# Kernel optimization log

Measured on AMD Instinct MI355X. Metric: run time of the kernel, lower is better.

The kernel has to match this reference:

```python
import jax, jax.numpy as jnp
import numpy as np
from jax import lax

V, E, H = 32000, 128, 128
B, T = 8, 512


def setup_inputs() -> dict:
    key = jax.random.key(0)
    ks = jax.random.split(key, 12)
    s = 1.0 / np.sqrt(H)
    return {
        "x": jax.random.randint(ks[0], (B, T), 0, V, dtype=jnp.int32),
        "embedding": jax.random.normal(ks[1], (V, E), jnp.float32) * s,
        "W_ih0": jax.random.normal(ks[2], (H, E), jnp.float32) * s,
        "W_hh0": jax.random.normal(ks[3], (H, H), jnp.float32) * s,
        "b_ih0": jax.random.normal(ks[4], (H,), jnp.float32) * s,
        "b_hh0": jax.random.normal(ks[5], (H,), jnp.float32) * s,
        "W_ih1": jax.random.normal(ks[6], (H, H), jnp.float32) * s,
        "W_hh1": jax.random.normal(ks[7], (H, H), jnp.float32) * s,
        "b_ih1": jax.random.normal(ks[8], (H,), jnp.float32) * s,
        "b_hh1": jax.random.normal(ks[9], (H,), jnp.float32) * s,
        "fc_W": jax.random.normal(ks[10], (V, H), jnp.float32) * s,
        "fc_b": jax.random.normal(ks[11], (V,), jnp.float32) * s,
    }


def _rnn_layer(x_tbe, W_ih, W_hh, b_ih, b_hh):
    # x_tbe: [T, B, in]. Precompute input contribution once (big GEMM), then scan.
    pre = jnp.einsum("tbe,he->tbh", x_tbe, W_ih) + b_ih + b_hh  # [T,B,H]

    def step(h, p):
        h = jnp.tanh(p + h @ W_hh.T)
        return h, h

    h0 = jnp.zeros((x_tbe.shape[1], W_hh.shape[0]), x_tbe.dtype)
    _, ys = lax.scan(step, h0, pre)
    return ys  # [T,B,H]


def reference(x, embedding, W_ih0, W_hh0, b_ih0, b_hh0,
              W_ih1, W_hh1, b_ih1, b_hh1, fc_W, fc_b):
    emb = embedding[x]                    # [B,T,E] gather
    h = jnp.transpose(emb, (1, 0, 2))     # [T,B,E] time-major for scan
    h = _rnn_layer(h, W_ih0, W_hh0, b_ih0, b_hh0)
    h = _rnn_layer(h, W_ih1, W_hh1, b_ih1, b_hh1)
    logits = jnp.einsum("tbh,vh->btv", h, fc_W) + fc_b  # [B,T,V]
    return logits
```

## Files before the change

kernel.cpp:

```cpp
#include <hip/hip_runtime.h>
#include <hip/hip_bf16.h>

typedef __attribute__((ext_vector_type(4))) float f32x4;
typedef __attribute__((ext_vector_type(4))) int   i32x4;
typedef __attribute__((ext_vector_type(8))) short s16x8;
typedef __attribute__((ext_vector_type(4))) unsigned short u16x4;
typedef __attribute__((ext_vector_type(2))) unsigned int  u32x2;
typedef __attribute__((ext_vector_type(2))) unsigned long long u64x2;

#define T_ 512
#define B_ 8
#define H_ 128
#define V_ 32000

#define WS_PRE0   0u
#define WS_H1B    (2u<<20)
#define WS_FCWB   (3u<<20)
#define WS_PIH    (11u<<20)
#define WS_FLAGS  (15u<<20)

__device__ __forceinline__ unsigned short f2b(float f) {
  unsigned int u = __float_as_uint(f);
  u = (u + 0x7FFFu + ((u >> 16) & 1u)) >> 16;
  return (unsigned short)u;
}

__device__ __forceinline__ float hsum4(f32x4 v) { return (v.x + v.y) + (v.z + v.w); }

__device__ __forceinline__ float tanh_fast(float x) {
  float e = __expf(2.f * x);
  return 1.f - 2.f * __builtin_amdgcn_rcpf(e + 1.f);
}

__device__ __forceinline__ f32x4 tanh4(f32x4 v) {
  f32x4 r;
  r.x = tanh_fast(v.x); r.y = tanh_fast(v.y);
  r.z = tanh_fast(v.z); r.w = tanh_fast(v.w);
  return r;
}

__device__ __forceinline__ u32x2 pk4(f32x4 v) {
  unsigned int a, b;
  asm("v_cvt_pk_bf16_f32 %0, %1, %2" : "=v"(a) : "v"(v.x), "v"(v.y));
  asm("v_cvt_pk_bf16_f32 %0, %1, %2" : "=v"(b) : "v"(v.z), "v"(v.w));
  u32x2 r; r.x = a; r.y = b; return r;
}

__device__ __forceinline__ void lds_barrier() {
  asm volatile("s_waitcnt lgkmcnt(0)\n\ts_barrier" ::: "memory");
}

__device__ __forceinline__ void st_u64(unsigned long long* p, unsigned long long v) {
  __hip_atomic_store(p, v, __ATOMIC_RELAXED, __HIP_MEMORY_SCOPE_AGENT);
}
__device__ __forceinline__ unsigned long long ld_u64(const unsigned long long* p) {
  return __hip_atomic_load(p, __ATOMIC_RELAXED, __HIP_MEMORY_SCOPE_AGENT);
}

#define MFMA16(A, B, C) __builtin_amdgcn_mfma_f32_16x16x32_bf16((A), (B), (C), 0, 0, 0)

__global__ __launch_bounds__(128) void pre_kernel(const float* __restrict__ emb,
                                                  const int* __restrict__ x,
                                                  const float* __restrict__ W,
                                                  const float* __restrict__ b1,
                                                  const float* __restrict__ b2,
                                                  float* __restrict__ out) {
  const int tid = threadIdx.x;
  __shared__ alignas(16) float lds_in[H_];
  f32x4 w[32];
#pragma unroll
  for (int r = 0; r < 32; ++r) w[r] = *(const f32x4*)(W + tid * H_ + 4 * r);
  const float bsum = b1[tid] + b2[tid];
  const int m0 = blockIdx.x * 16;

  auto src_row = [&](int m) -> const float* {
    int t = m >> 3, b = m & 7;
    int tok = x[(b << 9) + t];
    return emb + (size_t)tok * H_;
  };

  float stage = src_row(m0)[tid];
  for (int rr = 0; rr < 16; ++rr) {
    const int m = m0 + rr;
    lds_in[tid] = stage;
    __syncthreads();
    if (rr + 1 < 16) stage = src_row(m0 + rr + 1)[tid];
    f32x4 acc4 = {0.f, 0.f, 0.f, 0.f};
#pragma unroll
    for (int r = 0; r < 32; ++r) {
      f32x4 hv = *(const f32x4*)(lds_in + 4 * r);
      acc4 = __builtin_elementwise_fma(hv, w[r], acc4);
    }
    out[m * H_ + tid] = hsum4(acc4) + bsum;
    __syncthreads();
  }
}

__global__ __launch_bounds__(512) __attribute__((amdgpu_waves_per_eu(2, 2)))
void fused_scan5(const float* __restrict__ pre0,
                 const float* __restrict__ W_hh0,
                 const float* __restrict__ W_ih1,
                 const float* __restrict__ W_hh1,
                 const float* __restrict__ b_ih1,
                 const float* __restrict__ b_hh1,
                 unsigned short* __restrict__ h1b,
                 unsigned long long* __restrict__ pih_g,
                 unsigned int* __restrict__ prog1,
                 const float* __restrict__ fcw_src,
                 unsigned short* __restrict__ fcw_dst) {
  const int bid = blockIdx.x;
  const int tid = threadIdx.x;

  if (bid >= 2) {
    int idx = (bid - 2) * 512 + tid;
    const int stride = 64 * 512;
    const int n4 = V_ * H_ / 4;
    for (int c = idx; c < n4; c += stride) {
      f32x4 v = ((const f32x4*)fcw_src)[c];
      u16x4 o; o.x = f2b(v.x); o.y = f2b(v.y); o.z = f2b(v.z); o.w = f2b(v.w);
      ((u16x4*)fcw_dst)[c] = o;
    }
    return;
  }

  __shared__ unsigned short hl[2][16][136];
  const int wv = tid >> 6, lane = tid & 63;
  const int n = lane & 15, g = lane >> 4;
  const int nn = (n < 8) ? n : 7;
  for (int i = tid; i < 2 * 16 * 136; i += 512) ((unsigned short*)hl)[i] = 0;

  if (bid == 0) {
    const bool is0 = wv < 4;
    const int w = wv & 3, m0 = w * 32;
    const float* Wm = is0 ? W_hh0 : W_ih1;
    s16x8 whi[2][4], wlo[2][4];
#pragma unroll
    for (int hf = 0; hf < 2; ++hf)
#pragma unroll
      for (int kt = 0; kt < 4; ++kt) {
        const float* src = Wm + (m0 + hf * 16 + n) * H_ + kt * 32 + g * 8;
        s16x8 hi, lo;
#pragma unroll
        for (int j = 0; j < 8; ++j) {
          float v = src[j];
          unsigned short hb = f2b(v);
          hi[j] = (short)hb;
          lo[j] = (short)f2b(v - __uint_as_float(((unsigned int)hb) << 16));
        }
        whi[hf][kt] = hi; wlo[hf][kt] = lo;
      }
    f32x4 c0b = {0.f,0.f,0.f,0.f}, c1b = {0.f,0.f,0.f,0.f};
    if (!is0) {
      c0b = *(const f32x4*)(b_ih1 + m0 + g * 4) + *(const f32x4*)(b_hh1 + m0 + g * 4);
      c1b = *(const f32x4*)(b_ih1 + m0 + 16 + g * 4) + *(const f32x4*)(b_hh1 + m0 + 16 + g * 4);
    }
    f32x4 fif[4][2];
    if (is0) {
#pragma unroll
      for (int k = 0; k < 4; ++k) {
        fif[k][0] = *(const f32x4*)(pre0 + (k * B_ + nn) * H_ + m0 + g * 4);
        fif[k][1] = *(const f32x4*)(pre0 + (k * B_ + nn) * H_ + m0 + 16 + g * 4);
      }
    }
    __syncthreads();

    for (int base = 0; base < T_; base += 4) {
#pragma unroll
      for (int k = 0; k < 4; ++k) {
        const int s = base + k;
        const int rd = (k + 1) & 1, wr = k & 1;
        const unsigned short* hb = &hl[rd][n][0];
        s16x8 b0 = *(const s16x8*)(hb + g * 8);
        s16x8 b1 = *(const s16x8*)(hb + 32 + g * 8);
        s16x8 b2 = *(const s16x8*)(hb + 64 + g * 8);
        s16x8 b3 = *(const s16x8*)(hb + 96 + g * 8);
        if (is0) {
          f32x4 aH0 = fif[k][0], aL0 = {0.f,0.f,0.f,0.f};
          f32x4 aH1 = fif[k][1], aL1 = {0.f,0.f,0.f,0.f};
          aH0 = MFMA16(whi[0][0], b0, aH0); aL0 = MFMA16(wlo[0][0], b0, aL0);
          aH0 = MFMA16(whi[0][1], b1, aH0); aL0 = MFMA16(wlo[0][1], b1, aL0);
          aH0 = MFMA16(whi[0][2], b2, aH0); aL0 = MFMA16(wlo[0][2], b2, aL0);
          aH0 = MFMA16(whi[0][3], b3, aH0); aL0 = MFMA16(wlo[0][3], b3, aL0);
          aH1 = MFMA16(whi[1][0], b0, aH1); aL1 = MFMA16(wlo[1][0], b0, aL1);
          aH1 = MFMA16(whi[1][1], b1, aH1); aL1 = MFMA16(wlo[1][1], b1, aL1);
          aH1 = MFMA16(whi[1][2], b2, aH1); aL1 = MFMA16(wlo[1][2], b2, aL1);
          aH1 = MFMA16(whi[1][3], b3, aH1); aL1 = MFMA16(wlo[1][3], b3, aL1);
          f32x4 v0 = tanh4(aH0 + aL0), v1 = tanh4(aH1 + aL1);
          *(u32x2*)&hl[wr][n][m0 + g * 4] = pk4(v0);
          *(u32x2*)&hl[wr][n][m0 + 16 + g * 4] = pk4(v1);
          int sp = s + 4; if (sp > T_ - 1) sp = T_ - 1;
          fif[k][0] = *(const f32x4*)(pre0 + (sp * B_ + nn) * H_ + m0 + g * 4);
          fif[k][1] = *(const f32x4*)(pre0 + (sp * B_ + nn) * H_ + m0 + 16 + g * 4);
        } else {
          if (k == 0 && base >= 4 && lane == 0)
            __hip_atomic_fetch_add(prog1, 4u, __ATOMIC_RELEASE, __HIP_MEMORY_SCOPE_AGENT);
          if (s >= 1) {
            f32x4 v0 = c0b, v1 = c1b;
            v0 = MFMA16(whi[0][0], b0, v0); v1 = MFMA16(whi[1][0], b0, v1);
            v0 = MFMA16(whi[0][1], b1, v0); v1 = MFMA16(whi[1][1], b1, v1);
            v0 = MFMA16(whi[0][2], b2, v0); v1 = MFMA16(whi[1][2], b2, v1);
            v0 = MFMA16(whi[0][3], b3, v0); v1 = MFMA16(whi[1][3], b3, v1);
            u64x2 u0 = __builtin_bit_cast(u64x2, v0);
            u64x2 u1 = __builtin_bit_cast(u64x2, v1);
            unsigned long long* p0 = pih_g + ((size_t)((s - 1) * 8 + 2 * w) * 64 + lane) * 2;
            st_u64(p0, u0.x); st_u64(p0 + 1, u0.y);
            unsigned long long* p1 = pih_g + ((size_t)((s - 1) * 8 + 2 * w + 1) * 64 + lane) * 2;
            st_u64(p1, u1.x); st_u64(p1 + 1, u1.y);
          }
        }
        lds_barrier();
      }
    }
    if (!is0) {
      const unsigned short* hb = &hl[1][n][0];
      s16x8 b0 = *(const s16x8*)(hb + g * 8);
      s16x8 b1 = *(const s16x8*)(hb + 32 + g * 8);
      s16x8 b2 = *(const s16x8*)(hb + 64 + g * 8);
      s16x8 b3 = *(const s16x8*)(hb + 96 + g * 8);
      f32x4 v0 = c0b, v1 = c1b;
      v0 = MFMA16(whi[0][0], b0, v0); v1 = MFMA16(whi[1][0], b0, v1);
      v0 = MFMA16(whi[0][1], b1, v0); v1 = MFMA16(whi[1][1], b1, v1);
      v0 = MFMA16(whi[0][2], b2, v0); v1 = MFMA16(whi[1][2], b2, v1);
      v0 = MFMA16(whi[0][3], b3, v0); v1 = MFMA16(whi[1][3], b3, v1);
      u64x2 u0 = __builtin_bit_cast(u64x2, v0);
      u64x2 u1 = __builtin_bit_cast(u64x2, v1);
      unsigned long long* p0 = pih_g + ((size_t)(511 * 8 + 2 * w) * 64 + lane) * 2;
      st_u64(p0, u0.x); st_u64(p0 + 1, u0.y);
      unsigned long long* p1 = pih_g + ((size_t)(511 * 8 + 2 * w + 1) * 64 + lane) * 2;
      st_u64(p1, u1.x); st_u64(p1 + 1, u1.y);
      if (lane == 0)
        __hip_atomic_fetch_add(prog1, 16u, __ATOMIC_RELEASE, __HIP_MEMORY_SCOPE_AGENT);
    }
  } else {
    const int m0 = wv * 16;
    s16x8 whi[4], wlo[4];
#pragma unroll
    for (int kt = 0; kt < 4; ++kt) {
      const float* src = W_hh1 + (m0 + n) * H_ + kt * 32 + g * 8;
      s16x8 hi, lo;
#pragma unroll
      for (int j = 0; j < 8; ++j) {
        float v = src[j];
        unsigned short hb = f2b(v);
        hi[j] = (short)hb;
        lo[j] = (short)f2b(v - __uint_as_float(((unsigned int)hb) << 16));
      }
      whi[kt] = hi; wlo[kt] = lo;
    }
    __syncthreads();

    auto ld_pih = [&](int step) -> f32x4 {
      const unsigned long long* p = pih_g + ((size_t)(step * 8 + wv) * 64 + lane) * 2;
      u64x2 u; u.x = ld_u64(p); u.y = ld_u64(p + 1);
      return __builtin_bit_cast(f32x4, u);
    };
    while (__hip_atomic_load(prog1, __ATOMIC_ACQUIRE, __HIP_MEMORY_SCOPE_AGENT) < 20u)
      __builtin_amdgcn_s_sleep(2);
    f32x4 fif[4];
#pragma unroll
    for (int k = 0; k < 4; ++k) fif[k] = ld_pih(k);

    for (int base = 0; base < T_; base += 4) {
      if (base + 4 < T_) {
        const unsigned int t = 4u * (unsigned)(base + 9);
        while (__hip_atomic_load(prog1, __ATOMIC_ACQUIRE, __HIP_MEMORY_SCOPE_AGENT) < t)
          __builtin_amdgcn_s_sleep(2);
      }
#pragma unroll
      for (int k = 0; k < 4; ++k) {
        const int j = base + k;
        const int rd = (k + 1) & 1, wr = k & 1;
        const unsigned short* hb = &hl[rd][n][0];
        s16x8 b0 = *(const s16x8*)(hb + g * 8);
        s16x8 b1 = *(const s16x8*)(hb + 32 + g * 8);
        s16x8 b2 = *(const s16x8*)(hb + 64 + g * 8);
        s16x8 b3 = *(const s16x8*)(hb + 96 + g * 8);
        f32x4 aH = fif[k], aL = {0.f,0.f,0.f,0.f};
        aH = MFMA16(whi[0], b0, aH); aL = MFMA16(wlo[0], b0, aL);
        aH = MFMA16(whi[1], b1, aH); aL = MFMA16(wlo[1], b1, aL);
        aH = MFMA16(whi[2], b2, aH); aL = MFMA16(wlo[2], b2, aL);
        aH = MFMA16(whi[3], b3, aH); aL = MFMA16(wlo[3], b3, aL);
        f32x4 v = tanh4(aH + aL);
        u32x2 o = pk4(v);
        *(u32x2*)&hl[wr][n][m0 + g * 4] = o;
        if (n < 8) *(u32x2*)(h1b + ((j * B_ + n) << 7) + m0 + g * 4) = o;
        if (j + 4 < T_) fif[k] = ld_pih(j + 4);
        lds_barrier();
      }
    }
  }
}

__device__ __forceinline__ int swz(int row, int cc) {
  return row * 256 + ((cc ^ (row & 7)) << 4);
}

__global__ __launch_bounds__(256) void final_gemm5(const unsigned short* __restrict__ fcWb,
                                                   const unsigned short* __restrict__ h1b,
                                                   const float* __restrict__ bias,
                                                   float* __restrict__ out) {
  const int bid = blockIdx.x;
  const int x   = bid & 7;
  const int jb  = bid >> 3;
  const int mt  = jb & 31;
  const int ntl = jb >> 5;
  const int nt  = x * 32 + ntl;
  if (nt >= 250) return;

  __shared__ alignas(16) char smem[33792];
  const int tid = threadIdx.x;
  const int bb = mt >> 2, tb = mt & 3;
  const int t0 = tb << 7;
  const int v0 = nt << 7;
  const int lane = tid & 63, wvv = tid >> 6;

  const char* gW = (const char*)fcWb + (size_t)v0 * 256;
#pragma unroll
  for (int it = 0; it < 8; ++it) {
    int cidx = it * 256 + tid;
    i32x4 vw = *(const i32x4*)(gW + cidx * 16);
    *(i32x4*)(smem + swz(cidx >> 4, cidx & 15)) = vw;
  }
  __syncthreads();

  const int l15 = lane & 15, lg = lane >> 4;
  f32x4 acc[8][2] = {};
#pragma unroll
  for (int kk = 0; kk < 4; ++kk) {
    const int cc = kk * 4 + lg;
    s16x8 a[8], bfr[2];
#pragma unroll
    for (int vf = 0; vf < 8; ++vf)
      a[vf] = *(const s16x8*)(smem + swz(vf * 16 + l15, cc));
#pragma unroll
    for (int mf = 0; mf < 2; ++mf) {
      int trow = t0 + wvv * 32 + mf * 16 + l15;
      bfr[mf] = *(const s16x8*)(h1b + (size_t)((trow << 3) + bb) * H_ + kk * 32 + lg * 8);
    }
#pragma unroll
    for (int vf = 0; vf < 8; ++vf)
#pragma unroll
      for (int mf = 0; mf < 2; ++mf)
        acc[vf][mf] = __builtin_amdgcn_mfma_f32_16x16x32_bf16(a[vf], bfr[mf], acc[vf][mf], 0, 0, 0);
  }

#pragma unroll
  for (int vf = 0; vf < 8; ++vf) {
    f32x4 bv = *(const f32x4*)(bias + v0 + vf * 16 + (lg << 2));
#pragma unroll
    for (int mf = 0; mf < 2; ++mf) acc[vf][mf] += bv;
  }

  float* tbf = (float*)smem;
#pragma unroll
  for (int p = 0; p < 2; ++p) {
    __syncthreads();
#pragma unroll
    for (int q = 0; q < 4; ++q) {
      const int vf = p * 4 + q;
#pragma unroll
      for (int mf = 0; mf < 2; ++mf) {
        int t = wvv * 32 + mf * 16 + l15;
        int vl = q * 16 + lg * 4;
        *(f32x4*)(tbf + t * 66 + vl) = acc[vf][mf];
      }
    }
    __syncthreads();
#pragma unroll
    for (int it = 0; it < 8; ++it) {
      int row = it * 16 + (tid >> 4);
      int col = (tid & 15) * 4;
      f32x4 val = *(const f32x4*)(tbf + row * 66 + col);
      const size_t off = (size_t)((bb << 9) + t0 + row) * V_ + v0 + p * 64 + col;
      __builtin_nontemporal_store(val, (f32x4*)(out + off));
    }
  }
}

extern "C" void kernel_launch(void* const* d_in, const int* in_sizes, int n_in,
                              void* d_out, int out_size, void* d_ws, size_t ws_size,
                              hipStream_t stream) {
  const int*   x     = (const int*)d_in[0];
  const float* emb   = (const float*)d_in[1];
  const float* W_ih0 = (const float*)d_in[2];
  const float* W_hh0 = (const float*)d_in[3];
  const float* b_ih0 = (const float*)d_in[4];
  const float* b_hh0 = (const float*)d_in[5];
  const float* W_ih1 = (const float*)d_in[6];
  const float* W_hh1 = (const float*)d_in[7];
  const float* b_ih1 = (const float*)d_in[8];
  const float* b_hh1 = (const float*)d_in[9];
  const float* fc_W  = (const float*)d_in[10];
  const float* fc_b  = (const float*)d_in[11];
  float* out = (float*)d_out;

  char* ws = (char*)d_ws;
  float*              pre0  = (float*)(ws + WS_PRE0);
  unsigned short*     h1b   = (unsigned short*)(ws + WS_H1B);
  unsigned short*     fcWb  = (unsigned short*)(ws + WS_FCWB);
  unsigned long long* pih_g = (unsigned long long*)(ws + WS_PIH);
  unsigned int*       prog1 = (unsigned int*)(ws + WS_FLAGS);

  hipMemsetAsync(ws + WS_FLAGS, 0, 4096, stream);
  pre_kernel<<<256, 128, 0, stream>>>(emb, x, W_ih0, b_ih0, b_hh0, pre0);
  fused_scan5<<<66, 512, 0, stream>>>(pre0, W_hh0, W_ih1, W_hh1, b_ih1, b_hh1,
                                      h1b, pih_g, prog1, fc_W, fcWb);
  final_gemm5<<<8192, 256, 0, stream>>>(fcWb, h1b, fc_b, out);
}
```

Before: 475.4 us.

## Split recurrent scan into three pipelined blocks and convert fc weights in GEMM

The fused scan kernel now runs three blocks. Block 0 computes layer-0 recurrence alone with all 8 waves, block 1 computes the layer-1 input projection from h0 in global memory, and block 2 runs the layer-1 recurrence, all chained through acquire/release progress flags checked every 8 steps. This removes the layer-1 projection from the critical serial path of layer 0 and halves the per-wave MFMA chain. The separate fc_W fp32-to-bf16 conversion blocks are removed and the conversion moves into the final GEMM's tile load, which trades a workspace pass for redundant per-tile conversion across the 32 M-tiles.

```diff
diff --git a/kernel.cpp b/kernel.cpp
--- a/kernel.cpp
+++ b/kernel.cpp
@@ -6,7 +6,6 @@
 typedef __attribute__((ext_vector_type(8))) short s16x8;
 typedef __attribute__((ext_vector_type(4))) unsigned short u16x4;
 typedef __attribute__((ext_vector_type(2))) unsigned int  u32x2;
-typedef __attribute__((ext_vector_type(2))) unsigned long long u64x2;
 
 #define T_ 512
 #define B_ 8
@@ -15,9 +14,9 @@
 
 #define WS_PRE0   0u
 #define WS_H1B    (2u<<20)
-#define WS_FCWB   (3u<<20)
-#define WS_PIH    (11u<<20)
-#define WS_FLAGS  (15u<<20)
+#define WS_H0G    (3u<<20)
+#define WS_PIH    (4u<<20)
+#define WS_FLAGS  (8u<<20)
 
 __device__ __forceinline__ unsigned short f2b(float f) {
   unsigned int u = __float_as_uint(f);
@@ -50,14 +49,15 @@
   asm volatile("s_waitcnt lgkmcnt(0)\n\ts_barrier" ::: "memory");
 }
 
-__device__ __forceinline__ void st_u64(unsigned long long* p, unsigned long long v) {
-  __hip_atomic_store(p, v, __ATOMIC_RELAXED, __HIP_MEMORY_SCOPE_AGENT);
-}
-__device__ __forceinline__ unsigned long long ld_u64(const unsigned long long* p) {
-  return __hip_atomic_load(p, __ATOMIC_RELAXED, __HIP_MEMORY_SCOPE_AGENT);
+__device__ __forceinline__ unsigned int ld_flag_acq(const unsigned int* p) {
+  return __hip_atomic_load(p, __ATOMIC_ACQUIRE, __HIP_MEMORY_SCOPE_AGENT);
 }
 
 #define MFMA16(A, B, C) __builtin_amdgcn_mfma_f32_16x16x32_bf16((A), (B), (C), 0, 0, 0)
+
+__device__ __forceinline__ int swz(int row, int cc) {
+  return row * 256 + ((cc ^ (row & 7)) << 4);
+}
 
 __global__ __launch_bounds__(128) void pre_kernel(const float* __restrict__ emb,
                                                   const int* __restrict__ x,
@@ -96,143 +96,167 @@
   }
 }
 
+#define S0_STEP(S, FIF) { \
+  const int s_ = (S); \
+  const int rd = (s_ + 1) & 1, wr = s_ & 1; \
+  const unsigned short* hb = &hl[rd][n][0]; \
+  s16x8 b0 = *(const s16x8*)(hb + g * 8); \
+  s16x8 b1 = *(const s16x8*)(hb + 32 + g * 8); \
+  s16x8 b2 = *(const s16x8*)(hb + 64 + g * 8); \
+  s16x8 b3 = *(const s16x8*)(hb + 96 + g * 8); \
+  f32x4 ha = MFMA16(whi[0], b0, FIF); \
+  f32x4 hc = MFMA16(whi[2], b2, z4); \
+  f32x4 la = MFMA16(wlo[0], b0, z4); \
+  f32x4 lb = MFMA16(wlo[2], b2, z4); \
+  ha = MFMA16(whi[1], b1, ha); \
+  hc = MFMA16(whi[3], b3, hc); \
+  la = MFMA16(wlo[1], b1, la); \
+  lb = MFMA16(wlo[3], b3, lb); \
+  f32x4 v = tanh4((ha + hc) + (la + lb)); \
+  u32x2 o = pk4(v); \
+  *(u32x2*)&hl[wr][n][m0 + g * 4] = o; \
+  if (n < 8) *(u32x2*)(h0g + ((s_ * 8 + n) << 7) + m0 + g * 4) = o; \
+  int sp = s_ + 4; if (sp > T_ - 1) sp = T_ - 1; \
+  if ((s_ & 7) == 7) { \
+    asm volatile("s_waitcnt vmcnt(0)" ::: "memory"); \
+    (FIF) = *(const f32x4*)(pre0 + ((sp * 8 + nn) << 7) + m0 + g * 4); \
+    lds_barrier(); \
+    if (tid == 0) __hip_atomic_fetch_add(prog0, 8u, __ATOMIC_RELEASE, __HIP_MEMORY_SCOPE_AGENT); \
+  } else { \
+    (FIF) = *(const f32x4*)(pre0 + ((sp * 8 + nn) << 7) + m0 + g * 4); \
+    lds_barrier(); \
+  } \
+}
+
+#define S1_STEP(JJ, FB) { \
+  const int j_ = (JJ); \
+  f32x4 aa = MFMA16(whi[0], FB[0], biasD); \
+  f32x4 ab = MFMA16(whi[2], FB[2], z4); \
+  aa = MFMA16(whi[1], FB[1], aa); \
+  ab = MFMA16(whi[3], FB[3], ab); \
+  f32x4 v = aa + ab; \
+  *(f32x4*)(pih_gf + (size_t)(j_ * 8 + wv) * 64 + n * 4 + g) = v; \
+  if ((j_ & 7) == 7) { \
+    asm volatile("s_waitcnt vmcnt(0)" ::: "memory"); \
+    lds_barrier(); \
+    if (tid == 0) __hip_atomic_fetch_add(prog1, 8u, __ATOMIC_RELEASE, __HIP_MEMORY_SCOPE_AGENT); \
+  } \
+  int jp = j_ + 4; \
+  if (jp < T_) { \
+    const unsigned short* hsrc = h0g + ((jp * 8 + nn) << 7); \
+    FB[0] = *(const s16x8*)(hsrc + g * 8); \
+    FB[1] = *(const s16x8*)(hsrc + 32 + g * 8); \
+    FB[2] = *(const s16x8*)(hsrc + 64 + g * 8); \
+    FB[3] = *(const s16x8*)(hsrc + 96 + g * 8); \
+  } \
+}
+
+#define S2_STEP(J, PF) { \
+  const int j_ = (J); \
+  const int rd = (j_ + 1) & 1, wr = j_ & 1; \
+  const unsigned short* hb = &hl[rd][n][0]; \
+  s16x8 b0 = *(const s16x8*)(hb + g * 8); \
+  s16x8 b1 = *(const s16x8*)(hb + 32 + g * 8); \
+  s16x8 b2 = *(const s16x8*)(hb + 64 + g * 8); \
+  s16x8 b3 = *(const s16x8*)(hb + 96 + g * 8); \
+  f32x4 ha = MFMA16(whi[0], b0, PF); \
+  f32x4 hc = MFMA16(whi[2], b2, z4); \
+  f32x4 la = MFMA16(wlo[0], b0, z4); \
+  f32x4 lb = MFMA16(wlo[2], b2, z4); \
+  ha = MFMA16(whi[1], b1, ha); \
+  hc = MFMA16(whi[3], b3, hc); \
+  la = MFMA16(wlo[1], b1, la); \
+  lb = MFMA16(wlo[3], b3, lb); \
+  f32x4 v = tanh4((ha + hc) + (la + lb)); \
+  u32x2 o = pk4(v); \
+  *(u32x2*)&hl[wr][n][m0 + g * 4] = o; \
+  if (n < 8) *(u32x2*)(h1b + ((j_ * 8 + n) << 7) + m0 + g * 4) = o; \
+  int jp = j_ + 4; \
+  if (jp < T_) (PF) = *(const f32x4*)(pih_gf + (size_t)(jp * 8 + wv) * 64 + n * 4 + g); \
+  lds_barrier(); \
+}
+
 __global__ __launch_bounds__(512) __attribute__((amdgpu_waves_per_eu(2, 2)))
-void fused_scan5(const float* __restrict__ pre0,
+void fused_scan6(const float* __restrict__ pre0,
                  const float* __restrict__ W_hh0,
                  const float* __restrict__ W_ih1,
                  const float* __restrict__ W_hh1,
                  const float* __restrict__ b_ih1,
                  const float* __restrict__ b_hh1,
+                 unsigned short* __restrict__ h0g,
+                 float* __restrict__ pih_raw,
                  unsigned short* __restrict__ h1b,
-                 unsigned long long* __restrict__ pih_g,
-                 unsigned int* __restrict__ prog1,
-                 const float* __restrict__ fcw_src,
-                 unsigned short* __restrict__ fcw_dst) {
+                 unsigned int* __restrict__ prog0,
+                 unsigned int* __restrict__ prog1) {
   const int bid = blockIdx.x;
   const int tid = threadIdx.x;
-
-  if (bid >= 2) {
-    int idx = (bid - 2) * 512 + tid;
-    const int stride = 64 * 512;
-    const int n4 = V_ * H_ / 4;
-    for (int c = idx; c < n4; c += stride) {
-      f32x4 v = ((const f32x4*)fcw_src)[c];
-      u16x4 o; o.x = f2b(v.x); o.y = f2b(v.y); o.z = f2b(v.z); o.w = f2b(v.w);
-      ((u16x4*)fcw_dst)[c] = o;
-    }
-    return;
-  }
-
-  __shared__ unsigned short hl[2][16][136];
   const int wv = tid >> 6, lane = tid & 63;
   const int n = lane & 15, g = lane >> 4;
   const int nn = (n < 8) ? n : 7;
+  const int m0 = wv * 16;
+  const f32x4 z4 = {0.f, 0.f, 0.f, 0.f};
+  f32x4* pih_gf = (f32x4*)pih_raw;
+
+  __shared__ unsigned short hl[2][16][136];
   for (int i = tid; i < 2 * 16 * 136; i += 512) ((unsigned short*)hl)[i] = 0;
 
   if (bid == 0) {
-    const bool is0 = wv < 4;
-    const int w = wv & 3, m0 = w * 32;
-    const float* Wm = is0 ? W_hh0 : W_ih1;
-    s16x8 whi[2][4], wlo[2][4];
-#pragma unroll
-    for (int hf = 0; hf < 2; ++hf)
-#pragma unroll
-      for (int kt = 0; kt < 4; ++kt) {
-        const float* src = Wm + (m0 + hf * 16 + n) * H_ + kt * 32 + g * 8;
-        s16x8 hi, lo;
-#pragma unroll
-        for (int j = 0; j < 8; ++j) {
-          float v = src[j];
-          unsigned short hb = f2b(v);
-          hi[j] = (short)hb;
-          lo[j] = (short)f2b(v - __uint_as_float(((unsigned int)hb) << 16));
-        }
-        whi[hf][kt] = hi; wlo[hf][kt] = lo;
+    s16x8 whi[4], wlo[4];
+#pragma unroll
+    for (int kt = 0; kt < 4; ++kt) {
+      const float* src = W_hh0 + (m0 + n) * H_ + kt * 32 + g * 8;
+      s16x8 hi, lo;
+#pragma unroll
+      for (int j = 0; j < 8; ++j) {
+        float v = src[j];
+        unsigned short hb16 = f2b(v);
+        hi[j] = (short)hb16;
+        lo[j] = (short)f2b(v - __uint_as_float(((unsigned int)hb16) << 16));
       }
-    f32x4 c0b = {0.f,0.f,0.f,0.f}, c1b = {0.f,0.f,0.f,0.f};
-    if (!is0) {
-      c0b = *(const f32x4*)(b_ih1 + m0 + g * 4) + *(const f32x4*)(b_hh1 + m0 + g * 4);
-      c1b = *(const f32x4*)(b_ih1 + m0 + 16 + g * 4) + *(const f32x4*)(b_hh1 + m0 + 16 + g * 4);
-    }
-    f32x4 fif[4][2];
-    if (is0) {
-#pragma unroll
-      for (int k = 0; k < 4; ++k) {
-        fif[k][0] = *(const f32x4*)(pre0 + (k * B_ + nn) * H_ + m0 + g * 4);
-        fif[k][1] = *(const f32x4*)(pre0 + (k * B_ + nn) * H_ + m0 + 16 + g * 4);
-      }
-    }
-    __syncthreads();
-
+      whi[kt] = hi; wlo[kt] = lo;
+    }
+    f32x4 f0 = *(const f32x4*)(pre0 + ((0 * 8 + nn) << 7) + m0 + g * 4);
+    f32x4 f1 = *(const f32x4*)(pre0 + ((1 * 8 + nn) << 7) + m0 + g * 4);
+    f32x4 f2 = *(const f32x4*)(pre0 + ((2 * 8 + nn) << 7) + m0 + g * 4);
+    f32x4 f3 = *(const f32x4*)(pre0 + ((3 * 8 + nn) << 7) + m0 + g * 4);
+    __syncthreads();
     for (int base = 0; base < T_; base += 4) {
-#pragma unroll
-      for (int k = 0; k < 4; ++k) {
-        const int s = base + k;
-        const int rd = (k + 1) & 1, wr = k & 1;
-        const unsigned short* hb = &hl[rd][n][0];
-        s16x8 b0 = *(const s16x8*)(hb + g * 8);
-        s16x8 b1 = *(const s16x8*)(hb + 32 + g * 8);
-        s16x8 b2 = *(const s16x8*)(hb + 64 + g * 8);
-        s16x8 b3 = *(const s16x8*)(hb + 96 + g * 8);
-        if (is0) {
-          f32x4 aH0 = fif[k][0], aL0 = {0.f,0.f,0.f,0.f};
-          f32x4 aH1 = fif[k][1], aL1 = {0.f,0.f,0.f,0.f};
-          aH0 = MFMA16(whi[0][0], b0, aH0); aL0 = MFMA16(wlo[0][0], b0, aL0);
-          aH0 = MFMA16(whi[0][1], b1, aH0); aL0 = MFMA16(wlo[0][1], b1, aL0);
-          aH0 = MFMA16(whi[0][2], b2, aH0); aL0 = MFMA16(wlo[0][2], b2, aL0);
-          aH0 = MFMA16(whi[0][3], b3, aH0); aL0 = MFMA16(wlo[0][3], b3, aL0);
-          aH1 = MFMA16(whi[1][0], b0, aH1); aL1 = MFMA16(wlo[1][0], b0, aL1);
-          aH1 = MFMA16(whi[1][1], b1, aH1); aL1 = MFMA16(wlo[1][1], b1, aL1);
-          aH1 = MFMA16(whi[1][2], b2, aH1); aL1 = MFMA16(wlo[1][2], b2, aL1);
-          aH1 = MFMA16(whi[1][3], b3, aH1); aL1 = MFMA16(wlo[1][3], b3, aL1);
-          f32x4 v0 = tanh4(aH0 + aL0), v1 = tanh4(aH1 + aL1);
-          *(u32x2*)&hl[wr][n][m0 + g * 4] = pk4(v0);
-          *(u32x2*)&hl[wr][n][m0 + 16 + g * 4] = pk4(v1);
-          int sp = s + 4; if (sp > T_ - 1) sp = T_ - 1;
-          fif[k][0] = *(const f32x4*)(pre0 + (sp * B_ + nn) * H_ + m0 + g * 4);
-          fif[k][1] = *(const f32x4*)(pre0 + (sp * B_ + nn) * H_ + m0 + 16 + g * 4);
-        } else {
-          if (k == 0 && base >= 4 && lane == 0)
-            __hip_atomic_fetch_add(prog1, 4u, __ATOMIC_RELEASE, __HIP_MEMORY_SCOPE_AGENT);
-          if (s >= 1) {
-            f32x4 v0 = c0b, v1 = c1b;
-            v0 = MFMA16(whi[0][0], b0, v0); v1 = MFMA16(whi[1][0], b0, v1);
-            v0 = MFMA16(whi[0][1], b1, v0); v1 = MFMA16(whi[1][1], b1, v1);
-            v0 = MFMA16(whi[0][2], b2, v0); v1 = MFMA16(whi[1][2], b2, v1);
-            v0 = MFMA16(whi[0][3], b3, v0); v1 = MFMA16(whi[1][3], b3, v1);
-            u64x2 u0 = __builtin_bit_cast(u64x2, v0);
-            u64x2 u1 = __builtin_bit_cast(u64x2, v1);
-            unsigned long long* p0 = pih_g + ((size_t)((s - 1) * 8 + 2 * w) * 64 + lane) * 2;
-            st_u64(p0, u0.x); st_u64(p0 + 1, u0.y);
-            unsigned long long* p1 = pih_g + ((size_t)((s - 1) * 8 + 2 * w + 1) * 64 + lane) * 2;
-            st_u64(p1, u1.x); st_u64(p1 + 1, u1.y);
-          }
-        }
-        lds_barrier();
-      }
-    }
-    if (!is0) {
-      const unsigned short* hb = &hl[1][n][0];
-      s16x8 b0 = *(const s16x8*)(hb + g * 8);
-      s16x8 b1 = *(const s16x8*)(hb + 32 + g * 8);
-      s16x8 b2 = *(const s16x8*)(hb + 64 + g * 8);
-      s16x8 b3 = *(const s16x8*)(hb + 96 + g * 8);
-      f32x4 v0 = c0b, v1 = c1b;
-      v0 = MFMA16(whi[0][0], b0, v0); v1 = MFMA16(whi[1][0], b0, v1);
-      v0 = MFMA16(whi[0][1], b1, v0); v1 = MFMA16(whi[1][1], b1, v1);
-      v0 = MFMA16(whi[0][2], b2, v0); v1 = MFMA16(whi[1][2], b2, v1);
-      v0 = MFMA16(whi[0][3], b3, v0); v1 = MFMA16(whi[1][3], b3, v1);
-      u64x2 u0 = __builtin_bit_cast(u64x2, v0);
-      u64x2 u1 = __builtin_bit_cast(u64x2, v1);
-      unsigned long long* p0 = pih_g + ((size_t)(511 * 8 + 2 * w) * 64 + lane) * 2;
-      st_u64(p0, u0.x); st_u64(p0 + 1, u0.y);
-      unsigned long long* p1 = pih_g + ((size_t)(511 * 8 + 2 * w + 1) * 64 + lane) * 2;
-      st_u64(p1, u1.x); st_u64(p1 + 1, u1.y);
-      if (lane == 0)
-        __hip_atomic_fetch_add(prog1, 16u, __ATOMIC_RELEASE, __HIP_MEMORY_SCOPE_AGENT);
+      S0_STEP(base + 0, f0)
+      S0_STEP(base + 1, f1)
+      S0_STEP(base + 2, f2)
+      S0_STEP(base + 3, f3)
+    }
+  } else if (bid == 1) {
+    s16x8 whi[4];
+#pragma unroll
+    for (int kt = 0; kt < 4; ++kt) {
+      const float* src = W_ih1 + (m0 + n) * H_ + kt * 32 + g * 8;
+      s16x8 hi;
+#pragma unroll
+      for (int j = 0; j < 8; ++j) hi[j] = (short)f2b(src[j]);
+      whi[kt] = hi;
+    }
+    const f32x4 biasD = *(const f32x4*)(b_ih1 + m0 + g * 4) +
+                        *(const f32x4*)(b_hh1 + m0 + g * 4);
+    __syncthreads();
+    while (ld_flag_acq(prog0) < 4u) __builtin_amdgcn_s_sleep(8);
+    s16x8 fbA[4], fbB[4], fbC[4], fbD[4];
+#pragma unroll
+    for (int kt = 0; kt < 4; ++kt) {
+      fbA[kt] = *(const s16x8*)(h0g + ((0 * 8 + nn) << 7) + kt * 32 + g * 8);
+      fbB[kt] = *(const s16x8*)(h0g + ((1 * 8 + nn) << 7) + kt * 32 + g * 8);
+      fbC[kt] = *(const s16x8*)(h0g + ((2 * 8 + nn) << 7) + kt * 32 + g * 8);
+      fbD[kt] = *(const s16x8*)(h0g + ((3 * 8 + nn) << 7) + kt * 32 + g * 8);
+    }
+    for (int base = 0; base < T_; base += 4) {
+      unsigned int req = (unsigned)(base + 8); if (req > 512u) req = 512u;
+      while (ld_flag_acq(prog0) < req) __builtin_amdgcn_s_sleep(8);
+      S1_STEP(base + 0, fbA)
+      S1_STEP(base + 1, fbB)
+      S1_STEP(base + 2, fbC)
+      S1_STEP(base + 3, fbD)
     }
   } else {
-    const int m0 = wv * 16;
     s16x8 whi[4], wlo[4];
 #pragma unroll
     for (int kt = 0; kt < 4; ++kt) {
@@ -241,61 +265,30 @@
 #pragma unroll
       for (int j = 0; j < 8; ++j) {
         float v = src[j];
-        unsigned short hb = f2b(v);
-        hi[j] = (short)hb;
-        lo[j] = (short)f2b(v - __uint_as_float(((unsigned int)hb) << 16));
+        unsigned short hb16 = f2b(v);
+        hi[j] = (short)hb16;
+        lo[j] = (short)f2b(v - __uint_as_float(((unsigned int)hb16) << 16));
       }
       whi[kt] = hi; wlo[kt] = lo;
     }
     __syncthreads();
-
-    auto ld_pih = [&](int step) -> f32x4 {
-      const unsigned long long* p = pih_g + ((size_t)(step * 8 + wv) * 64 + lane) * 2;
-      u64x2 u; u.x = ld_u64(p); u.y = ld_u64(p + 1);
-      return __builtin_bit_cast(f32x4, u);
-    };
-    while (__hip_atomic_load(prog1, __ATOMIC_ACQUIRE, __HIP_MEMORY_SCOPE_AGENT) < 20u)
-      __builtin_amdgcn_s_sleep(2);
-    f32x4 fif[4];
-#pragma unroll
-    for (int k = 0; k < 4; ++k) fif[k] = ld_pih(k);
-
+    while (ld_flag_acq(prog1) < 4u) __builtin_amdgcn_s_sleep(8);
+    f32x4 p0 = *(const f32x4*)(pih_gf + (size_t)(0 * 8 + wv) * 64 + n * 4 + g);
+    f32x4 p1 = *(const f32x4*)(pih_gf + (size_t)(1 * 8 + wv) * 64 + n * 4 + g);
+    f32x4 p2 = *(const f32x4*)(pih_gf + (size_t)(2 * 8 + wv) * 64 + n * 4 + g);
+    f32x4 p3 = *(const f32x4*)(pih_gf + (size_t)(3 * 8 + wv) * 64 + n * 4 + g);
     for (int base = 0; base < T_; base += 4) {
-      if (base + 4 < T_) {
-        const unsigned int t = 4u * (unsigned)(base + 9);
-        while (__hip_atomic_load(prog1, __ATOMIC_ACQUIRE, __HIP_MEMORY_SCOPE_AGENT) < t)
-          __builtin_amdgcn_s_sleep(2);
-      }
-#pragma unroll
-      for (int k = 0; k < 4; ++k) {
-        const int j = base + k;
-        const int rd = (k + 1) & 1, wr = k & 1;
-        const unsigned short* hb = &hl[rd][n][0];
-        s16x8 b0 = *(const s16x8*)(hb + g * 8);
-        s16x8 b1 = *(const s16x8*)(hb + 32 + g * 8);
-        s16x8 b2 = *(const s16x8*)(hb + 64 + g * 8);
-        s16x8 b3 = *(const s16x8*)(hb + 96 + g * 8);
-        f32x4 aH = fif[k], aL = {0.f,0.f,0.f,0.f};
-        aH = MFMA16(whi[0], b0, aH); aL = MFMA16(wlo[0], b0, aL);
-        aH = MFMA16(whi[1], b1, aH); aL = MFMA16(wlo[1], b1, aL);
-        aH = MFMA16(whi[2], b2, aH); aL = MFMA16(wlo[2], b2, aL);
-        aH = MFMA16(whi[3], b3, aH); aL = MFMA16(wlo[3], b3, aL);
-        f32x4 v = tanh4(aH + aL);
-        u32x2 o = pk4(v);
-        *(u32x2*)&hl[wr][n][m0 + g * 4] = o;
-        if (n < 8) *(u32x2*)(h1b + ((j * B_ + n) << 7) + m0 + g * 4) = o;
-        if (j + 4 < T_) fif[k] = ld_pih(j + 4);
-        lds_barrier();
-      }
-    }
-  }
-}
-
-__device__ __forceinline__ int swz(int row, int cc) {
-  return row * 256 + ((cc ^ (row & 7)) << 4);
-}
-
-__global__ __launch_bounds__(256) void final_gemm5(const unsigned short* __restrict__ fcWb,
+      unsigned int req = (unsigned)(base + 8); if (req > 512u) req = 512u;
+      while (ld_flag_acq(prog1) < req) __builtin_amdgcn_s_sleep(8);
+      S2_STEP(base + 0, p0)
+      S2_STEP(base + 1, p1)
+      S2_STEP(base + 2, p2)
+      S2_STEP(base + 3, p3)
+    }
+  }
+}
+
+__global__ __launch_bounds__(256) void final_gemm6(const float* __restrict__ fc_W,
                                                    const unsigned short* __restrict__ h1b,
                                                    const float* __restrict__ bias,
                                                    float* __restrict__ out) {
@@ -314,12 +307,16 @@
   const int v0 = nt << 7;
   const int lane = tid & 63, wvv = tid >> 6;
 
-  const char* gW = (const char*)fcWb + (size_t)v0 * 256;
 #pragma unroll
   for (int it = 0; it < 8; ++it) {
-    int cidx = it * 256 + tid;
-    i32x4 vw = *(const i32x4*)(gW + cidx * 16);
-    *(i32x4*)(smem + swz(cidx >> 4, cidx & 15)) = vw;
+    int c = it * 256 + tid;
+    int row = c >> 4, cc = c & 15;
+    const float* src = fc_W + (size_t)(v0 + row) * H_ + cc * 8;
+    f32x4 va = *(const f32x4*)src;
+    f32x4 vb = *(const f32x4*)(src + 4);
+    u32x2 pa = pk4(va), pb = pk4(vb);
+    i32x4 w16; w16.x = (int)pa.x; w16.y = (int)pa.y; w16.z = (int)pb.x; w16.w = (int)pb.y;
+    *(i32x4*)(smem + swz(row, cc)) = w16;
   }
   __syncthreads();
 
@@ -341,7 +338,7 @@
     for (int vf = 0; vf < 8; ++vf)
 #pragma unroll
       for (int mf = 0; mf < 2; ++mf)
-        acc[vf][mf] = __builtin_amdgcn_mfma_f32_16x16x32_bf16(a[vf], bfr[mf], acc[vf][mf], 0, 0, 0);
+        acc[vf][mf] = MFMA16(a[vf], bfr[mf], acc[vf][mf]);
   }
 
 #pragma unroll
@@ -395,15 +392,16 @@
   float* out = (float*)d_out;
 
   char* ws = (char*)d_ws;
-  float*              pre0  = (float*)(ws + WS_PRE0);
-  unsigned short*     h1b   = (unsigned short*)(ws + WS_H1B);
-  unsigned short*     fcWb  = (unsigned short*)(ws + WS_FCWB);
-  unsigned long long* pih_g = (unsigned long long*)(ws + WS_PIH);
-  unsigned int*       prog1 = (unsigned int*)(ws + WS_FLAGS);
+  float*          pre0  = (float*)(ws + WS_PRE0);
+  unsigned short* h1b   = (unsigned short*)(ws + WS_H1B);
+  unsigned short* h0g   = (unsigned short*)(ws + WS_H0G);
+  float*          pih   = (float*)(ws + WS_PIH);
+  unsigned int*   prog0 = (unsigned int*)(ws + WS_FLAGS);
+  unsigned int*   prog1 = (unsigned int*)(ws + WS_FLAGS + 64);
 
   hipMemsetAsync(ws + WS_FLAGS, 0, 4096, stream);
   pre_kernel<<<256, 128, 0, stream>>>(emb, x, W_ih0, b_ih0, b_hh0, pre0);
-  fused_scan5<<<66, 512, 0, stream>>>(pre0, W_hh0, W_ih1, W_hh1, b_ih1, b_hh1,
-                                      h1b, pih_g, prog1, fc_W, fcWb);
-  final_gemm5<<<8192, 256, 0, stream>>>(fcWb, h1b, fc_b, out);
-}
+  fused_scan6<<<3, 512, 0, stream>>>(pre0, W_hh0, W_ih1, W_hh1, b_ih1, b_hh1,
+                                     h0g, pih, h1b, prog0, prog1);
+  final_gemm6<<<8192, 256, 0, stream>>>(fc_W, h1b, fc_b, out);
+}
```

After: 547.0 us. +15.1%, slower.
